# Kernel tuning notes

Hardware: AMD Instinct MI355X
Metric: run time of the kernel (lower is better)

Reference implementation:

```python
import jax, jax.numpy as jnp
import numpy as np

N_PIX = 196608  # 12 * 128**2 (HEALPix nside=128)
F = 32          # filters (Fin == Fout for residual)
DM = 2          # depth multiplier


def _cheb_sep_conv(x, idx, wnb, wd, wp, b):
    """Separable Chebyshev graph conv.
    x: [B,N,F] maps; idx: [N,nb] neighbor indices; wnb: [N,nb] Laplacian weights;
    wd: [K,F,DM] depthwise Chebyshev weights; wp: [F*DM,Fout] pointwise; b: [Fout].
    """
    def L(t):  # sparse Laplacian apply via fixed-degree neighbor gather
        return jnp.einsum('bnjf,nj->bnf', t[:, idx, :], wnb)
    K = wd.shape[0]
    Ts = [x, L(x)]
    for _ in range(K - 2):  # Chebyshev recursion T_k = 2 L T_{k-1} - T_{k-2}
        Ts.append(2.0 * L(Ts[-1]) - Ts[-2])
    T = jnp.stack(Ts, 0)                      # [K,B,N,F]
    y = jnp.einsum('kbnf,kfd->bnfd', T, wd)   # depthwise over Chebyshev orders
    Bb, Nn, Ff, Dd = y.shape
    y = y.reshape(Bb, Nn, Ff * Dd)
    return y @ wp + b                         # pointwise mix to Fout


def _layernorm(x, gamma, beta, eps=1e-6):
    mu = jnp.mean(x, axis=-1, keepdims=True)
    var = jnp.mean(jnp.square(x - mu), axis=-1, keepdims=True)
    return (x - mu) * jax.lax.rsqrt(var + eps) * gamma + beta


def setup_inputs() -> dict:
    key = jax.random.key(0)
    ks = jax.random.split(key, 10)
    inp = {
        'maps': jax.random.normal(ks[0], (1, N_PIX, F), jnp.float32),
        'idx1': jax.random.randint(ks[1], (N_PIX, 8), 0, N_PIX, jnp.int32),
        'w1_nb': jax.random.normal(ks[2], (N_PIX, 8), jnp.float32) * 0.1,
        'idx2': jax.random.randint(ks[3], (N_PIX, 20), 0, N_PIX, jnp.int32),
        'w2_nb': jax.random.normal(ks[4], (N_PIX, 20), jnp.float32) * 0.1,
        'wd1': jax.random.normal(ks[5], (6, F, DM), jnp.float32) * 0.1,
        'wp1': jax.random.normal(ks[6], (F * DM, F), jnp.float32) * 0.1,
        'b1': jnp.zeros((F,), jnp.float32),
        'gamma1': jnp.ones((F,), jnp.float32),
        'beta1': jnp.zeros((F,), jnp.float32),
        'wd2': jax.random.normal(ks[7], (10, F, DM), jnp.float32) * 0.1,
        'wp2': jax.random.normal(ks[8], (F * DM, F), jnp.float32) * 0.1,
        'b2': jnp.zeros((F,), jnp.float32),
        'gamma2': jnp.ones((F,), jnp.float32),
        'beta2': jnp.zeros((F,), jnp.float32),
    }
    return inp


def reference(maps, idx1, w1_nb, idx2, w2_nb, wd1, wp1, b1, gamma1, beta1,
              wd2, wp2, b2, gamma2, beta2):
    res = maps
    x = _cheb_sep_conv(maps, idx1, w1_nb, wd1, wp1, b1)   # K=6, nb=8
    x = jax.nn.relu(x)
    x = _layernorm(x, gamma1, beta1)
    x = _cheb_sep_conv(x, idx2, w2_nb, wd2, wp2, b2)      # K=10, nb=20
    x = jax.nn.relu(x)
    x = _layernorm(x, gamma2, beta2)
    return x + res
```

## Files before the change

### kernel.cpp

```cpp
#include <hip/hip_runtime.h>

constexpr int NPIX = 196608;
constexpr int FF   = 32;
constexpr size_t SLOT = (size_t)NPIX * FF;

__device__ __forceinline__ float b2f(ushort u) {
    union { float f; unsigned int i; } v; v.i = ((unsigned int)u) << 16; return v.f;
}
__device__ __forceinline__ ushort f2b(float f) {
    union { float f; unsigned int i; } v; v.f = f;
    unsigned int r = v.i + 0x7fffu + ((v.i >> 16) & 1u);
    return (ushort)(r >> 16);
}

__global__ __launch_bounds__(256) void f2b_kernel(const float* __restrict__ src,
                                                  ushort* __restrict__ dst) {
    int i = (blockIdx.x * 256 + threadIdx.x) * 4;
    float4 v = *reinterpret_cast<const float4*>(src + i);
    ushort4 o;
    o.x = f2b(v.x); o.y = f2b(v.y); o.z = f2b(v.z); o.w = f2b(v.w);
    *reinterpret_cast<ushort4*>(dst + i) = o;
}

template<int NB>
__global__ __launch_bounds__(256) void cheb_init_kernel(
    const ushort* __restrict__ Tprev,
    const int*    __restrict__ idx,
    const float*  __restrict__ wnb,
    ushort*       __restrict__ Tout)
{
    int t = blockIdx.x * 256 + threadIdx.x;
    int n = t >> 5;
    int f = t & 31;
    const int4*   ip  = reinterpret_cast<const int4*>(idx + (size_t)n * NB);
    const float4* wp4 = reinterpret_cast<const float4*>(wnb + (size_t)n * NB);
    float s = 0.f;
#pragma unroll
    for (int j4 = 0; j4 < NB / 4; ++j4) {
        int4   i4 = ip[j4];
        float4 w4 = wp4[j4];
        s += w4.x * b2f(Tprev[(size_t)i4.x * FF + f]);
        s += w4.y * b2f(Tprev[(size_t)i4.y * FF + f]);
        s += w4.z * b2f(Tprev[(size_t)i4.z * FF + f]);
        s += w4.w * b2f(Tprev[(size_t)i4.w * FF + f]);
    }
    Tout[(size_t)n * FF + f] = f2b(s);
}

template<int NB>
__global__ __launch_bounds__(256) void cheb_step_kernel(
    const ushort* __restrict__ Tprev,
    const ushort* __restrict__ Told,
    ushort*       __restrict__ Tout,
    const int*    __restrict__ idx,
    const float*  __restrict__ wnb)
{
    int t = blockIdx.x * 256 + threadIdx.x;
    int n = t >> 5;
    int f = t & 31;
    const int4*   ip  = reinterpret_cast<const int4*>(idx + (size_t)n * NB);
    const float4* wp4 = reinterpret_cast<const float4*>(wnb + (size_t)n * NB);
    float s = 0.f;
#pragma unroll
    for (int j4 = 0; j4 < NB / 4; ++j4) {
        int4   i4 = ip[j4];
        float4 w4 = wp4[j4];
        s += w4.x * b2f(Tprev[(size_t)i4.x * FF + f]);
        s += w4.y * b2f(Tprev[(size_t)i4.y * FF + f]);
        s += w4.z * b2f(Tprev[(size_t)i4.z * FF + f]);
        s += w4.w * b2f(Tprev[(size_t)i4.w * FF + f]);
    }
    size_t base = (size_t)n * FF + f;
    Tout[base] = f2b(2.f * s - b2f(Told[base]));
}

template<int K, bool RESIDUAL, bool OUT_BF16>
__global__ __launch_bounds__(256) void finish_kernel(
    const ushort* __restrict__ chain,
    const float*  __restrict__ wd,
    const float*  __restrict__ wp,
    const float*  __restrict__ bias,
    const float*  __restrict__ gamma,
    const float*  __restrict__ beta,
    const float*  __restrict__ resid,
    void*         __restrict__ outp)
{
    __shared__ float swp[64 * 32];
    __shared__ float sacc[8 * 64];

    int tid = threadIdx.x;
    for (int i = tid; i < 64 * 32; i += 256) swp[i] = wp[i];

    int n  = tid >> 5;
    int f  = tid & 31;
    int n0 = blockIdx.x * 8;
    size_t base = (size_t)(n0 + n) * FF + f;

    float a0 = 0.f, a1 = 0.f;
#pragma unroll
    for (int k = 0; k < K; ++k) {
        float tv = b2f(chain[(size_t)k * SLOT + base]);
        float2 w = *reinterpret_cast<const float2*>(wd + (k * FF + f) * 2);
        a0 += tv * w.x;
        a1 += tv * w.y;
    }
    sacc[n * 64 + f * 2]     = a0;
    sacc[n * 64 + f * 2 + 1] = a1;
    __syncthreads();

    float z = bias[f];
#pragma unroll
    for (int u = 0; u < 64; ++u)
        z += sacc[n * 64 + u] * swp[u * 32 + f];
    z = fmaxf(z, 0.f);

    float s1 = z, s2 = z * z;
#pragma unroll
    for (int m = 16; m >= 1; m >>= 1) {
        s1 += __shfl_xor(s1, m, 32);
        s2 += __shfl_xor(s2, m, 32);
    }
    float mu  = s1 * (1.f / 32.f);
    float var = s2 * (1.f / 32.f) - mu * mu;
    float v = (z - mu) * rsqrtf(var + 1e-6f) * gamma[f] + beta[f];
    if (RESIDUAL) v += resid[base];

    if (OUT_BF16) ((ushort*)outp)[base] = f2b(v);
    else          ((float*)outp)[base]  = v;
}

extern "C" void kernel_launch(void* const* d_in, const int* in_sizes, int n_in,
                              void* d_out, int out_size, void* d_ws, size_t ws_size,
                              hipStream_t stream) {
    const float* maps = (const float*)d_in[0];
    const int*   idx1 = (const int*)  d_in[1];
    const float* w1nb = (const float*)d_in[2];
    const int*   idx2 = (const int*)  d_in[3];
    const float* w2nb = (const float*)d_in[4];
    const float* wd1  = (const float*)d_in[5];
    const float* wp1  = (const float*)d_in[6];
    const float* b1   = (const float*)d_in[7];
    const float* g1   = (const float*)d_in[8];
    const float* be1  = (const float*)d_in[9];
    const float* wd2  = (const float*)d_in[10];
    const float* wp2  = (const float*)d_in[11];
    const float* b2   = (const float*)d_in[12];
    const float* g2   = (const float*)d_in[13];
    const float* be2  = (const float*)d_in[14];
    float* out = (float*)d_out;

    ushort* slots = (ushort*)d_ws;
    ushort* B = slots;
    ushort* A = slots + 4 * SLOT;

    const int nodeBlocks = NPIX * FF / 256;
    const int cvtBlocks  = NPIX * FF / (256*4);
    const int finBlocks  = NPIX / 8;

    f2b_kernel<<<cvtBlocks, 256, 0, stream>>>(maps, A);
    cheb_init_kernel<8><<<nodeBlocks, 256, 0, stream>>>(A, idx1, w1nb, A + SLOT);
    cheb_step_kernel<8><<<nodeBlocks, 256, 0, stream>>>(A + SLOT,   A,          A + 2*SLOT, idx1, w1nb);
    cheb_step_kernel<8><<<nodeBlocks, 256, 0, stream>>>(A + 2*SLOT, A + SLOT,   A + 3*SLOT, idx1, w1nb);
    cheb_step_kernel<8><<<nodeBlocks, 256, 0, stream>>>(A + 3*SLOT, A + 2*SLOT, A + 4*SLOT, idx1, w1nb);
    cheb_step_kernel<8><<<nodeBlocks, 256, 0, stream>>>(A + 4*SLOT, A + 3*SLOT, A + 5*SLOT, idx1, w1nb);
    finish_kernel<6, false, true><<<finBlocks, 256, 0, stream>>>(A, wd1, wp1, b1, g1, be1, nullptr, B);

    cheb_init_kernel<20><<<nodeBlocks, 256, 0, stream>>>(B, idx2, w2nb, B + SLOT);
    for (int k = 2; k <= 9; ++k)
        cheb_step_kernel<20><<<nodeBlocks, 256, 0, stream>>>(
            B + (size_t)(k-1)*SLOT, B + (size_t)(k-2)*SLOT, B + (size_t)k*SLOT, idx2, w2nb);
    finish_kernel<10, true, false><<<finBlocks, 256, 0, stream>>>(B, wd2, wp2, b2, g2, be2, maps, out);
}
```

Baseline: 767.1 us.

## Pack two bf16 features per thread in Chebyshev steps; MFMA pointwise finish

The Chebyshev gather kernels now have each thread handle two adjacent features through a 32-bit load. This halves the thread count and the per-node reloads of index and weight data, and widens each gather access. The finish kernel is rewritten to compute the pointwise 64x32 mix with bf16 MFMA on 64-node tiles, with layernorm done in registers via shuffles. The trade-off is extra rounding, since the depthwise sums and pointwise weights are cast to bf16 before the matmul.

```diff
diff --git a/kernel.cpp b/kernel.cpp
--- a/kernel.cpp
+++ b/kernel.cpp
@@ -3,6 +3,9 @@
 constexpr int NPIX = 196608;
 constexpr int FF   = 32;
 constexpr size_t SLOT = (size_t)NPIX * FF;
+
+typedef short bf16x8 __attribute__((ext_vector_type(8)));
+typedef float f32x4  __attribute__((ext_vector_type(4)));
 
 __device__ __forceinline__ float b2f(ushort u) {
     union { float f; unsigned int i; } v; v.i = ((unsigned int)u) << 16; return v.f;
@@ -23,32 +26,35 @@
 }
 
 template<int NB>
-__global__ __launch_bounds__(256) void cheb_init_kernel(
+__global__ __launch_bounds__(256) void cheb_init2(
     const ushort* __restrict__ Tprev,
     const int*    __restrict__ idx,
     const float*  __restrict__ wnb,
     ushort*       __restrict__ Tout)
 {
     int t = blockIdx.x * 256 + threadIdx.x;
-    int n = t >> 5;
-    int f = t & 31;
+    int n = t >> 4;
+    int h = t & 15;
+    const uint*   Tp  = reinterpret_cast<const uint*>(Tprev);
     const int4*   ip  = reinterpret_cast<const int4*>(idx + (size_t)n * NB);
     const float4* wp4 = reinterpret_cast<const float4*>(wnb + (size_t)n * NB);
-    float s = 0.f;
+    float s0 = 0.f, s1 = 0.f;
 #pragma unroll
     for (int j4 = 0; j4 < NB / 4; ++j4) {
         int4   i4 = ip[j4];
         float4 w4 = wp4[j4];
-        s += w4.x * b2f(Tprev[(size_t)i4.x * FF + f]);
-        s += w4.y * b2f(Tprev[(size_t)i4.y * FF + f]);
-        s += w4.z * b2f(Tprev[(size_t)i4.z * FF + f]);
-        s += w4.w * b2f(Tprev[(size_t)i4.w * FF + f]);
-    }
-    Tout[(size_t)n * FF + f] = f2b(s);
+        uint u;
+        u = Tp[(size_t)i4.x * 16 + h]; s0 += w4.x * b2f((ushort)u); s1 += w4.x * b2f((ushort)(u >> 16));
+        u = Tp[(size_t)i4.y * 16 + h]; s0 += w4.y * b2f((ushort)u); s1 += w4.y * b2f((ushort)(u >> 16));
+        u = Tp[(size_t)i4.z * 16 + h]; s0 += w4.z * b2f((ushort)u); s1 += w4.z * b2f((ushort)(u >> 16));
+        u = Tp[(size_t)i4.w * 16 + h]; s0 += w4.w * b2f((ushort)u); s1 += w4.w * b2f((ushort)(u >> 16));
+    }
+    reinterpret_cast<uint*>(Tout)[(size_t)n * 16 + h] =
+        ((uint)f2b(s1) << 16) | (uint)f2b(s0);
 }
 
 template<int NB>
-__global__ __launch_bounds__(256) void cheb_step_kernel(
+__global__ __launch_bounds__(256) void cheb_step2(
     const ushort* __restrict__ Tprev,
     const ushort* __restrict__ Told,
     ushort*       __restrict__ Tout,
@@ -56,26 +62,31 @@
     const float*  __restrict__ wnb)
 {
     int t = blockIdx.x * 256 + threadIdx.x;
-    int n = t >> 5;
-    int f = t & 31;
+    int n = t >> 4;
+    int h = t & 15;
+    const uint*   Tp  = reinterpret_cast<const uint*>(Tprev);
     const int4*   ip  = reinterpret_cast<const int4*>(idx + (size_t)n * NB);
     const float4* wp4 = reinterpret_cast<const float4*>(wnb + (size_t)n * NB);
-    float s = 0.f;
+    float s0 = 0.f, s1 = 0.f;
 #pragma unroll
     for (int j4 = 0; j4 < NB / 4; ++j4) {
         int4   i4 = ip[j4];
         float4 w4 = wp4[j4];
-        s += w4.x * b2f(Tprev[(size_t)i4.x * FF + f]);
-        s += w4.y * b2f(Tprev[(size_t)i4.y * FF + f]);
-        s += w4.z * b2f(Tprev[(size_t)i4.z * FF + f]);
-        s += w4.w * b2f(Tprev[(size_t)i4.w * FF + f]);
-    }
-    size_t base = (size_t)n * FF + f;
-    Tout[base] = f2b(2.f * s - b2f(Told[base]));
+        uint u;
+        u = Tp[(size_t)i4.x * 16 + h]; s0 += w4.x * b2f((ushort)u); s1 += w4.x * b2f((ushort)(u >> 16));
+        u = Tp[(size_t)i4.y * 16 + h]; s0 += w4.y * b2f((ushort)u); s1 += w4.y * b2f((ushort)(u >> 16));
+        u = Tp[(size_t)i4.z * 16 + h]; s0 += w4.z * b2f((ushort)u); s1 += w4.z * b2f((ushort)(u >> 16));
+        u = Tp[(size_t)i4.w * 16 + h]; s0 += w4.w * b2f((ushort)u); s1 += w4.w * b2f((ushort)(u >> 16));
+    }
+    size_t base = (size_t)n * 16 + h;
+    uint to = reinterpret_cast<const uint*>(Told)[base];
+    float t0 = 2.f * s0 - b2f((ushort)to);
+    float t1 = 2.f * s1 - b2f((ushort)(to >> 16));
+    reinterpret_cast<uint*>(Tout)[base] = ((uint)f2b(t1) << 16) | (uint)f2b(t0);
 }
 
 template<int K, bool RESIDUAL, bool OUT_BF16>
-__global__ __launch_bounds__(256) void finish_kernel(
+__global__ __launch_bounds__(256) void finish_mfma(
     const ushort* __restrict__ chain,
     const float*  __restrict__ wd,
     const float*  __restrict__ wp,
@@ -85,48 +96,87 @@
     const float*  __restrict__ resid,
     void*         __restrict__ outp)
 {
-    __shared__ float swp[64 * 32];
-    __shared__ float sacc[8 * 64];
+    __shared__ __align__(16) ushort sA[4][16][72];
+    __shared__ __align__(16) ushort sB[32][72];
 
     int tid = threadIdx.x;
-    for (int i = tid; i < 64 * 32; i += 256) swp[i] = wp[i];
-
-    int n  = tid >> 5;
-    int f  = tid & 31;
-    int n0 = blockIdx.x * 8;
-    size_t base = (size_t)(n0 + n) * FF + f;
-
-    float a0 = 0.f, a1 = 0.f;
-#pragma unroll
-    for (int k = 0; k < K; ++k) {
-        float tv = b2f(chain[(size_t)k * SLOT + base]);
-        float2 w = *reinterpret_cast<const float2*>(wd + (k * FF + f) * 2);
-        a0 += tv * w.x;
-        a1 += tv * w.y;
-    }
-    sacc[n * 64 + f * 2]     = a0;
-    sacc[n * 64 + f * 2 + 1] = a1;
+    int w = tid >> 6;
+    int l = tid & 63;
+
+    for (int i = tid; i < 64 * 32; i += 256) {
+        int u = i >> 5, g = i & 31;
+        sB[g][u] = f2b(wp[i]);
+    }
+
+    int nbase = blockIdx.x * 64 + w * 16;
+
+#pragma unroll
+    for (int p = 0; p < 8; ++p) {
+        int flat = p * 64 + l;
+        int nloc = flat >> 5;
+        int f    = flat & 31;
+        size_t base = (size_t)(nbase + nloc) * FF + f;
+        float a0 = 0.f, a1 = 0.f;
+#pragma unroll
+        for (int k = 0; k < K; ++k) {
+            float tv = b2f(chain[(size_t)k * SLOT + base]);
+            float2 wk = *reinterpret_cast<const float2*>(wd + (k * FF + f) * 2);
+            a0 += tv * wk.x;
+            a1 += tv * wk.y;
+        }
+        uint packed = ((uint)f2b(a1) << 16) | (uint)f2b(a0);
+        reinterpret_cast<uint*>(&sA[w][nloc][0])[f] = packed;
+    }
     __syncthreads();
 
-    float z = bias[f];
-#pragma unroll
-    for (int u = 0; u < 64; ++u)
-        z += sacc[n * 64 + u] * swp[u * 32 + f];
-    z = fmaxf(z, 0.f);
-
-    float s1 = z, s2 = z * z;
-#pragma unroll
-    for (int m = 16; m >= 1; m >>= 1) {
-        s1 += __shfl_xor(s1, m, 32);
-        s2 += __shfl_xor(s2, m, 32);
-    }
-    float mu  = s1 * (1.f / 32.f);
-    float var = s2 * (1.f / 32.f) - mu * mu;
-    float v = (z - mu) * rsqrtf(var + 1e-6f) * gamma[f] + beta[f];
-    if (RESIDUAL) v += resid[base];
-
-    if (OUT_BF16) ((ushort*)outp)[base] = f2b(v);
-    else          ((float*)outp)[base]  = v;
+    f32x4 acc0 = {0.f, 0.f, 0.f, 0.f};
+    f32x4 acc1 = {0.f, 0.f, 0.f, 0.f};
+    int r  = l & 15;
+    int ko = (l >> 4) * 8;
+#pragma unroll
+    for (int kt = 0; kt < 2; ++kt) {
+        bf16x8 aF = *reinterpret_cast<const bf16x8*>(&sA[w][r][kt * 32 + ko]);
+        bf16x8 b0 = *reinterpret_cast<const bf16x8*>(&sB[r][kt * 32 + ko]);
+        bf16x8 b1 = *reinterpret_cast<const bf16x8*>(&sB[16 + r][kt * 32 + ko]);
+        acc0 = __builtin_amdgcn_mfma_f32_16x16x32_bf16(aF, b0, acc0, 0, 0, 0);
+        acc1 = __builtin_amdgcn_mfma_f32_16x16x32_bf16(aF, b1, acc1, 0, 0, 0);
+    }
+
+    float bias_lo = bias[r],  bias_hi = bias[16 + r];
+    float gam_lo  = gamma[r], gam_hi  = gamma[16 + r];
+    float bet_lo  = beta[r],  bet_hi  = beta[16 + r];
+
+#pragma unroll
+    for (int v = 0; v < 4; ++v) {
+        acc0[v] = fmaxf(acc0[v] + bias_lo, 0.f);
+        acc1[v] = fmaxf(acc1[v] + bias_hi, 0.f);
+    }
+#pragma unroll
+    for (int v = 0; v < 4; ++v) {
+        float s1 = acc0[v] + acc1[v];
+        float s2 = acc0[v] * acc0[v] + acc1[v] * acc1[v];
+#pragma unroll
+        for (int m = 1; m < 16; m <<= 1) {
+            s1 += __shfl_xor(s1, m);
+            s2 += __shfl_xor(s2, m);
+        }
+        float mu  = s1 * (1.f / 32.f);
+        float var = s2 * (1.f / 32.f) - mu * mu;
+        float rs  = rsqrtf(var + 1e-6f);
+        int n = nbase + (l >> 4) * 4 + v;
+        size_t o0 = (size_t)n * FF + r;
+        size_t o1 = o0 + 16;
+        float z0 = (acc0[v] - mu) * rs * gam_lo + bet_lo;
+        float z1 = (acc1[v] - mu) * rs * gam_hi + bet_hi;
+        if (RESIDUAL) { z0 += resid[o0]; z1 += resid[o1]; }
+        if (OUT_BF16) {
+            ((ushort*)outp)[o0] = f2b(z0);
+            ((ushort*)outp)[o1] = f2b(z1);
+        } else {
+            ((float*)outp)[o0] = z0;
+            ((float*)outp)[o1] = z1;
+        }
+    }
 }
 
 extern "C" void kernel_launch(void* const* d_in, const int* in_sizes, int n_in,
@@ -153,21 +203,22 @@
     ushort* B = slots;
     ushort* A = slots + 4 * SLOT;
 
-    const int nodeBlocks = NPIX * FF / 256;
-    const int cvtBlocks  = NPIX * FF / (256*4);
-    const int finBlocks  = NPIX / 8;
+    const int stepBlocks = NPIX * 16 / 256;
+    const int cvtBlocks  = NPIX * FF / (256 * 4);
+    const int finBlocks  = NPIX / 64;
 
     f2b_kernel<<<cvtBlocks, 256, 0, stream>>>(maps, A);
-    cheb_init_kernel<8><<<nodeBlocks, 256, 0, stream>>>(A, idx1, w1nb, A + SLOT);
-    cheb_step_kernel<8><<<nodeBlocks, 256, 0, stream>>>(A + SLOT,   A,          A + 2*SLOT, idx1, w1nb);
-    cheb_step_kernel<8><<<nodeBlocks, 256, 0, stream>>>(A + 2*SLOT, A + SLOT,   A + 3*SLOT, idx1, w1nb);
-    cheb_step_kernel<8><<<nodeBlocks, 256, 0, stream>>>(A + 3*SLOT, A + 2*SLOT, A + 4*SLOT, idx1, w1nb);
-    cheb_step_kernel<8><<<nodeBlocks, 256, 0, stream>>>(A + 4*SLOT, A + 3*SLOT, A + 5*SLOT, idx1, w1nb);
-    finish_kernel<6, false, true><<<finBlocks, 256, 0, stream>>>(A, wd1, wp1, b1, g1, be1, nullptr, B);
-
-    cheb_init_kernel<20><<<nodeBlocks, 256, 0, stream>>>(B, idx2, w2nb, B + SLOT);
+    cheb_init2<8><<<stepBlocks, 256, 0, stream>>>(A, idx1, w1nb, A + SLOT);
+    cheb_step2<8><<<stepBlocks, 256, 0, stream>>>(A + SLOT,     A,              A + 2 * SLOT, idx1, w1nb);
+    cheb_step2<8><<<stepBlocks, 256, 0, stream>>>(A + 2 * SLOT, A + SLOT,       A + 3 * SLOT, idx1, w1nb);
+    cheb_step2<8><<<stepBlocks, 256, 0, stream>>>(A + 3 * SLOT, A + 2 * SLOT,   A + 4 * SLOT, idx1, w1nb);
+    cheb_step2<8><<<stepBlocks, 256, 0, stream>>>(A + 4 * SLOT, A + 3 * SLOT,   A + 5 * SLOT, idx1, w1nb);
+    finish_mfma<6, false, true><<<finBlocks, 256, 0, stream>>>(A, wd1, wp1, b1, g1, be1, nullptr, B);
+
+    cheb_init2<20><<<stepBlocks, 256, 0, stream>>>(B, idx2, w2nb, B + SLOT);
     for (int k = 2; k <= 9; ++k)
-        cheb_step_kernel<20><<<nodeBlocks, 256, 0, stream>>>(
-            B + (size_t)(k-1)*SLOT, B + (size_t)(k-2)*SLOT, B + (size_t)k*SLOT, idx2, w2nb);
-    finish_kernel<10, true, false><<<finBlocks, 256, 0, stream>>>(B, wd2, wp2, b2, g2, be2, maps, out);
-}
+        cheb_step2<20><<<stepBlocks, 256, 0, stream>>>(
+            B + (size_t)(k - 1) * SLOT, B + (size_t)(k - 2) * SLOT,
+            B + (size_t)k * SLOT, idx2, w2nb);
+    finish_mfma<10, true, false><<<finBlocks, 256, 0, stream>>>(B, wd2, wp2, b2, g2, be2, maps, out);
+}
```

Measured after the change: 733.7 us. 1.05x faster.
